# Kernel tuning notes

Hardware: AMD Instinct MI355X
Metric: run time of the kernel (lower is better)

The kernel has to match this reference:

```python
import jax, jax.numpy as jnp
import numpy as np

NB_CLASSES = 4
MRG = 0.05
ALPHA = 32.0
CL_W = 0.05
Z_PRUNE = 0.3
EPS = 1e-12


def _proxy_anchor(X, labels, valid, P):
    # X: [N, D] flattened span-pair features; labels: [N] int; valid: [N] float mask; P: [C, D]
    Xn = X / jnp.maximum(jnp.linalg.norm(X, axis=1, keepdims=True), EPS)
    Pn = P / jnp.maximum(jnp.linalg.norm(P, axis=1, keepdims=True), EPS)
    cos = Xn @ Pn.T  # [N, C]
    onehot = jax.nn.one_hot(labels, NB_CLASSES, dtype=cos.dtype)
    p_hot = onehot * valid[:, None]
    n_hot = (1.0 - onehot) * valid[:, None]
    pos_exp = jnp.exp(-ALPHA * (cos - MRG))
    neg_exp = jnp.exp(ALPHA * (cos + MRG))
    P_sim_sum = (p_hot * pos_exp).sum(axis=0)  # [C]
    N_sim_sum = (n_hot * neg_exp).sum(axis=0)  # [C]
    num_valid = jnp.maximum((p_hot.sum(axis=0) > 0).sum(), 1).astype(cos.dtype)
    pos_term = jnp.log1p(P_sim_sum).sum() / num_valid
    neg_term = jnp.log1p(N_sim_sum).sum() / NB_CLASSES
    return pos_term + neg_term


def _cl_loss(table, labels, attention_mask, P):
    B, L = table.shape[0], table.shape[1]
    lens = attention_mask.sum(axis=1)  # [B]
    idx = jnp.arange(L)
    rv = (idx[None, :] >= 1) & (idx[None, :] < (lens[:, None] - 1))  # [B, L]
    valid = (rv[:, :, None] & rv[:, None, :]).reshape(B, L * L).astype(table.dtype)
    X = table.reshape(B, L * L, -1)
    lab = labels.reshape(B, L * L)
    per_sample = jax.vmap(lambda x, l, v: _proxy_anchor(x, l, v, P))(X, lab, valid)
    return (CL_W * per_sample).mean()


def _span_pruning(pred, z, attention_mask):
    B = attention_mask.shape[0]
    mask_len = attention_mask.sum(axis=1) - 2
    length = (mask_len.astype(jnp.float32) * z).astype(jnp.int32)
    length = jnp.maximum(length, 10)
    length = jnp.minimum(length, mask_len * mask_len)
    pred_sort = -jnp.sort(-pred.reshape(B, -1), axis=1)  # descending
    topkth = pred_sort[jnp.arange(B), length - 1]
    return pred >= topkth[:, None, None]


def setup_inputs() -> dict:
    key = jax.random.key(0)
    ks = jax.random.split(key, 8)
    B, L, D = 4, 128, 768
    return {
        "table_edge": jax.random.normal(ks[0], (B, L, L, D), dtype=jnp.float32),
        "table_senti": jax.random.normal(ks[1], (B, L, L, D), dtype=jnp.float32),
        "attention_mask": jnp.ones((B, L), dtype=jnp.int32),
        "table_labels_S": jax.random.randint(ks[2], (B, L, L), 0, 2, dtype=jnp.int32),
        "table_labels_E": jax.random.randint(ks[3], (B, L, L), 0, 2, dtype=jnp.int32),
        "labels_edge": jax.random.randint(ks[4], (B, L, L), 0, 4, dtype=jnp.int32),
        "labels_senti": jax.random.randint(ks[5], (B, L, L), 0, 4, dtype=jnp.int32),
        "proxies_edge": jax.random.normal(ks[6], (4, D), dtype=jnp.float32),
        "proxies_senti": jax.random.normal(ks[7], (4, D), dtype=jnp.float32),
        "w_S": jax.random.normal(jax.random.fold_in(key, 10), (D,), dtype=jnp.float32) * 0.02,
        "b_S": jnp.zeros((1,), dtype=jnp.float32),
        "w_E": jax.random.normal(jax.random.fold_in(key, 11), (D,), dtype=jnp.float32) * 0.02,
        "b_E": jnp.zeros((1,), dtype=jnp.float32),
        "ID": 1,
        "epoch": 1,
    }


def reference(table_edge, table_senti, attention_mask, table_labels_S, table_labels_E,
              labels_edge, labels_senti, proxies_edge, proxies_senti,
              w_S, b_S, w_E, b_E, ID, epoch):
    cl_edge = _cl_loss(table_edge, labels_edge, attention_mask, proxies_edge)
    cl_senti = _cl_loss(table_senti, labels_senti, attention_mask, proxies_senti)

    logits_S = jnp.einsum('blmd,d->blm', table_edge, w_S) + b_S[0]
    logits_E = jnp.einsum('blmd,d->blm', table_edge, w_E) + b_E[0]

    weight = (table_labels_S >= 0).astype(logits_S.dtype)
    tS = table_labels_S.astype(logits_S.dtype)
    tE = table_labels_E.astype(logits_E.dtype)
    # BCEWithLogits: softplus(x) - x*t, weighted, mean over all elements
    loss_S = (weight * (jax.nn.softplus(logits_S) - logits_S * tS)).mean()
    loss_E = (weight * (jax.nn.softplus(logits_E) - logits_E * tE)).mean()

    S_pred = jax.nn.sigmoid(logits_S) * weight
    E_pred = jax.nn.sigmoid(logits_E) * weight
    pred_S = _span_pruning(S_pred, Z_PRUNE, attention_mask)
    pred_E = _span_pruning(E_pred, Z_PRUNE, attention_mask)

    return cl_edge, cl_senti, loss_S, loss_E, pred_S, pred_E
```

## Files before the change

kernel.cpp:

```cpp
#include <hip/hip_runtime.h>
#include <math.h>

#define LSEQ 128
#define NLL 16384
#define NBATCH 4
#define DIM 768
#define NB 4
#define ALPHA_C 32.0f
#define MRG_C 0.05f
#define CLW_C 0.05f
#define BPB 256
#define KS 24

__device__ __forceinline__ float wave_reduce_f(float v) {
#pragma unroll
    for (int s = 1; s < 64; s <<= 1) v += __shfl_xor(v, s);
    return v;
}

__device__ __forceinline__ float dot4(float4 a, float4 b) {
    return a.x*b.x + a.y*b.y + a.z*b.z + a.w*b.w;
}

template<bool EDGE>
__device__ __forceinline__ void kloop2(const float* __restrict__ rp0,
                                       const float* __restrict__ rp1,
                                       const float* __restrict__ wlds, int sub,
                                       float& xx0, float& d00, float& d01, float& d02, float& d03,
                                       float& dS0, float& dE0,
                                       float& xx1, float& d10, float& d11, float& d12, float& d13,
                                       float& dS1, float& dE1)
{
#pragma unroll 4
    for (int k = 0; k < KS; ++k) {
        const int off = k*32 + sub*4;
        const float4 x0 = *reinterpret_cast<const float4*>(rp0 + off);
        const float4 x1 = *reinterpret_cast<const float4*>(rp1 + off);
        const float4 w0 = *reinterpret_cast<const float4*>(&wlds[0*DIM + off]);
        const float4 w1 = *reinterpret_cast<const float4*>(&wlds[1*DIM + off]);
        const float4 w2 = *reinterpret_cast<const float4*>(&wlds[2*DIM + off]);
        const float4 w3 = *reinterpret_cast<const float4*>(&wlds[3*DIM + off]);
        xx0 += dot4(x0,x0); d00 += dot4(x0,w0); d01 += dot4(x0,w1); d02 += dot4(x0,w2); d03 += dot4(x0,w3);
        xx1 += dot4(x1,x1); d10 += dot4(x1,w0); d11 += dot4(x1,w1); d12 += dot4(x1,w2); d13 += dot4(x1,w3);
        if constexpr (EDGE) {
            const float4 w4 = *reinterpret_cast<const float4*>(&wlds[4*DIM + off]);
            const float4 w5 = *reinterpret_cast<const float4*>(&wlds[5*DIM + off]);
            dS0 += dot4(x0,w4); dE0 += dot4(x0,w5);
            dS1 += dot4(x1,w4); dE1 += dot4(x1,w5);
        }
    }
}

__global__ __launch_bounds__(256)
void fused_pass(const float* __restrict__ tabE, const float* __restrict__ tabS,
                const int* __restrict__ labE, const int* __restrict__ labSen,
                const int* __restrict__ attn,
                const float* __restrict__ proxE, const float* __restrict__ proxSen,
                const float* __restrict__ wS, const float* __restrict__ bS,
                const float* __restrict__ wE, const float* __restrict__ bE,
                const int* __restrict__ tlabS, const int* __restrict__ tlabE,
                float* __restrict__ pS, float* __restrict__ pE,
                float* __restrict__ partE, float* __restrict__ partSen)
{
    __shared__ float wlds[6*DIM];
    __shared__ float red[7*64];

    const int tid = threadIdx.x, wib = tid >> 6, lane = tid & 63;
    const int tbl = blockIdx.x >> 10;
    const int g = blockIdx.x & 1023;
    const int row0 = g << 6;
    const int b = g >> 8;
    const bool EDGE = (tbl == 0);

    const float* table = EDGE ? tabE : tabS;
    const float* prox  = EDGE ? proxE : proxSen;
    const int NW = EDGE ? 6 : 4;

    for (int i2 = tid; i2 < NW*192; i2 += 256) {
        const int v = i2 / 192, e = (i2 % 192) * 4;
        const float* src = (v < 4) ? (prox + v*DIM + e) : ((v == 4) ? (wS + e) : (wE + e));
        *reinterpret_cast<float4*>(&wlds[v*DIM + e]) = *reinterpret_cast<const float4*>(src);
    }
    __syncthreads();

    const int rgrp = lane >> 3, sub = lane & 7;
    const int r0 = row0 + wib*16 + rgrp*2;
    const float* rp0 = table + (size_t)r0 * DIM;
    const float* rp1 = rp0 + DIM;

    float xx0=0,d00=0,d01=0,d02=0,d03=0,dS0=0,dE0=0;
    float xx1=0,d10=0,d11=0,d12=0,d13=0,dS1=0,dE1=0;
    if (EDGE) kloop2<true >(rp0,rp1,wlds,sub,xx0,d00,d01,d02,d03,dS0,dE0,xx1,d10,d11,d12,d13,dS1,dE1);
    else      kloop2<false>(rp0,rp1,wlds,sub,xx0,d00,d01,d02,d03,dS0,dE0,xx1,d10,d11,d12,d13,dS1,dE1);

#pragma unroll
    for (int s = 1; s < 8; s <<= 1) {
        xx0+=__shfl_xor(xx0,s); d00+=__shfl_xor(d00,s); d01+=__shfl_xor(d01,s);
        d02+=__shfl_xor(d02,s); d03+=__shfl_xor(d03,s); dS0+=__shfl_xor(dS0,s); dE0+=__shfl_xor(dE0,s);
        xx1+=__shfl_xor(xx1,s); d10+=__shfl_xor(d10,s); d11+=__shfl_xor(d11,s);
        d12+=__shfl_xor(d12,s); d13+=__shfl_xor(d13,s); dS1+=__shfl_xor(dS1,s); dE1+=__shfl_xor(dE1,s);
    }
    if (sub == 0) {
        const int rr = wib*16 + rgrp*2;
        *reinterpret_cast<float2*>(&red[0*64+rr]) = make_float2(xx0, xx1);
        *reinterpret_cast<float2*>(&red[1*64+rr]) = make_float2(d00, d10);
        *reinterpret_cast<float2*>(&red[2*64+rr]) = make_float2(d01, d11);
        *reinterpret_cast<float2*>(&red[3*64+rr]) = make_float2(d02, d12);
        *reinterpret_cast<float2*>(&red[4*64+rr]) = make_float2(d03, d13);
        *reinterpret_cast<float2*>(&red[5*64+rr]) = make_float2(dS0, dS1);
        *reinterpret_cast<float2*>(&red[6*64+rr]) = make_float2(dE0, dE1);
    }
    __syncthreads();
    if (wib != 0) return;

    int lens_i = attn[b*LSEQ + lane] + attn[b*LSEQ + 64 + lane];
#pragma unroll
    for (int s = 1; s < 64; s <<= 1) lens_i += __shfl_xor(lens_i, s);

    float pinv[NB];
#pragma unroll
    for (int c = 0; c < NB; ++c) {
        float s2 = 0.f;
#pragma unroll
        for (int t = 0; t < 12; ++t) { const float w = wlds[c*DIM + t*64 + lane]; s2 += w*w; }
        s2 = wave_reduce_f(s2);
        pinv[c] = 1.0f / fmaxf(sqrtf(s2), 1e-12f);
    }

    const int r = row0 + lane;
    const float xx = red[lane];
    float dd[NB] = { red[64+lane], red[128+lane], red[192+lane], red[256+lane] };
    const float xinv = 1.0f / fmaxf(sqrtf(xx), 1e-12f);
    const int i = r & (NLL - 1);
    const int l = i >> 7, m = i & (LSEQ - 1);
    const bool valid = (l >= 1) && (l < lens_i - 1) && (m >= 1) && (m < lens_i - 1);
    const int lab = (EDGE ? labE : labSen)[r];

    float Pa[NB] = {0,0,0,0}, Na[NB] = {0,0,0,0}, Ca[NB] = {0,0,0,0};
    if (valid) {
#pragma unroll
        for (int c = 0; c < NB; ++c) {
            const float cs = dd[c] * xinv * pinv[c];
            if (lab == c) { Pa[c] = expf(-ALPHA_C * (cs - MRG_C)); Ca[c] = 1.f; }
            else          { Na[c] = expf( ALPHA_C * (cs + MRG_C)); }
        }
    }
    float sBS = 0.f, sBE = 0.f;
    if (EDGE) {
        const float dS = red[320+lane], dE = red[384+lane];
        const float xSl = dS + bS[0], xEl = dE + bE[0];
        const int ls = tlabS[r], le = tlabE[r];
        const float w = (ls >= 0) ? 1.f : 0.f;
        const float spS = fmaxf(xSl, 0.f) + log1pf(expf(-fabsf(xSl)));
        const float spE = fmaxf(xEl, 0.f) + log1pf(expf(-fabsf(xEl)));
        sBS = w * (spS - xSl * (float)ls);
        sBE = w * (spE - xEl * (float)le);
        pS[r] = w / (1.f + expf(-xSl));
        pE[r] = w / (1.f + expf(-xEl));
    }

#pragma unroll
    for (int c = 0; c < NB; ++c) {
        Pa[c] = wave_reduce_f(Pa[c]); Na[c] = wave_reduce_f(Na[c]); Ca[c] = wave_reduce_f(Ca[c]);
    }
    sBS = wave_reduce_f(sBS); sBE = wave_reduce_f(sBE);

    if (lane == 0) {
        float* pp = EDGE ? partE : partSen;
        const int blk = g & (BPB - 1);
        const int base = b * 14;
#pragma unroll
        for (int c = 0; c < NB; ++c) {
            pp[(base + c)     * BPB + blk] = Pa[c];
            pp[(base + 4 + c) * BPB + blk] = Na[c];
            pp[(base + 8 + c) * BPB + blk] = Ca[c];
        }
        pp[(base + 12) * BPB + blk] = sBS;
        pp[(base + 13) * BPB + blk] = sBE;
    }
}

__global__ __launch_bounds__(1024)
void tail_k(const float* __restrict__ pS, const float* __restrict__ pE,
            const int* __restrict__ attn,
            const float* __restrict__ partE, const float* __restrict__ partS,
            float* __restrict__ out)
{
    __shared__ unsigned sh[NLL];
    __shared__ int csum[16];
    __shared__ float gg[56];
    const int tid = threadIdx.x, wave = tid >> 6, lane = tid & 63;

    if (blockIdx.x >= 8) {
        const int tbl = blockIdx.x - 8;
        const float* part = (tbl == 0) ? partE : partS;
        for (int grp = wave; grp < 56; grp += 16) {
            float s = 0.f;
#pragma unroll
            for (int j = lane; j < BPB; j += 64) s += part[grp*BPB + j];
            s = wave_reduce_f(s);
            if (lane == 0) gg[grp] = s;
        }
        __syncthreads();
        if (tid == 0) {
            float tot = 0.f;
            for (int b = 0; b < NBATCH; ++b) {
                const float* G = gg + b * 14;
                int nv = 0;
                for (int c = 0; c < NB; ++c) nv += (G[8+c] > 0.f) ? 1 : 0;
                const float nvf = (float)((nv > 1) ? nv : 1);
                float pos = 0.f, neg = 0.f;
                for (int c = 0; c < NB; ++c) { pos += log1pf(G[c]); neg += log1pf(G[4+c]); }
                tot += pos / nvf + neg * 0.25f;
            }
            out[tbl] = CLW_C * tot * 0.25f;
            if (tbl == 0) {
                float bs = 0.f, be = 0.f;
                for (int b = 0; b < NBATCH; ++b) { bs += gg[b*14 + 12]; be += gg[b*14 + 13]; }
                out[2] = bs * (1.0f / 65536.0f);
                out[3] = be * (1.0f / 65536.0f);
            }
        }
        return;
    }

    const int a = blockIdx.x >> 2;
    const int b = blockIdx.x & 3;
    const float* p = (a ? pE : pS) + (size_t)b * NLL;
    float* o = out + 4 + (size_t)a * (NBATCH * NLL) + (size_t)b * NLL;

    int asum = attn[b*LSEQ + lane] + attn[b*LSEQ + 64 + lane];
#pragma unroll
    for (int s = 1; s < 64; s <<= 1) asum += __shfl_xor(asum, s);
    const int mask_len = asum - 2;
    int k = (int)((float)mask_len * 0.3f);
    k = (k > 10) ? k : 10;
    const int ml2 = mask_len * mask_len;
    k = (k < ml2) ? k : ml2;

    for (int j = tid; j < NLL; j += 1024) sh[j] = __float_as_uint(p[j]);
    __syncthreads();

    unsigned lo = 0u, hi = 0xFFFFFFFFu;
    for (int it = 0; it < 32; ++it) {
        if (lo >= hi) break;
        const unsigned span = hi - lo;
        const unsigned mid = lo + (span >> 1) + (span & 1u);
        int c = 0;
        for (int j = tid; j < NLL; j += 1024) c += (sh[j] >= mid) ? 1 : 0;
#pragma unroll
        for (int s = 1; s < 64; s <<= 1) c += __shfl_xor(c, s);
        if (lane == 0) csum[wave] = c;
        __syncthreads();
        int tot = 0;
#pragma unroll
        for (int w = 0; w < 16; ++w) tot += csum[w];
        if (tot >= k) lo = mid; else hi = mid - 1u;
        __syncthreads();
    }

    for (int j = tid; j < NLL; j += 1024) o[j] = (sh[j] >= lo) ? 1.0f : 0.0f;
}

extern "C" void kernel_launch(void* const* d_in, const int* in_sizes, int n_in,
                              void* d_out, int out_size, void* d_ws, size_t ws_size,
                              hipStream_t stream)
{
    const float* table_edge  = (const float*)d_in[0];
    const float* table_senti = (const float*)d_in[1];
    const int*   attn        = (const int*)d_in[2];
    const int*   tlabS       = (const int*)d_in[3];
    const int*   tlabE       = (const int*)d_in[4];
    const int*   lab_edge    = (const int*)d_in[5];
    const int*   lab_senti   = (const int*)d_in[6];
    const float* prox_edge   = (const float*)d_in[7];
    const float* prox_senti  = (const float*)d_in[8];
    const float* w_S         = (const float*)d_in[9];
    const float* b_S         = (const float*)d_in[10];
    const float* w_E         = (const float*)d_in[11];
    const float* b_E         = (const float*)d_in[12];

    float* out   = (float*)d_out;
    float* ws    = (float*)d_ws;
    float* pS    = ws;
    float* pE    = ws + 65536;
    float* partE = ws + 131072;
    float* partS = partE + 14336;

    fused_pass<<<2048, 256, 0, stream>>>(table_edge, table_senti,
        lab_edge, lab_senti, attn, prox_edge, prox_senti,
        w_S, b_S, w_E, b_E, tlabS, tlabE, pS, pE, partE, partS);
    tail_k<<<10, 1024, 0, stream>>>(pS, pE, attn, partE, partS, out);
}
```

Before: 109.4 us.

## Process four rows per lane group, 128 rows per block, per-wave epilogue

Each 8-lane group now accumulates four rows instead of two, so each block covers 128 rows and the grid halves to 1024 blocks. Edge and senti blocks are interleaved by block index. The post-processing now runs in every wave on its own 32 rows, and the four waves' partial sums are combined through shared memory before one write per block. The aim is to reuse each LDS weight load across more rows and to spread the epilogue across all waves instead of one. In exchange, register pressure is higher (launch bounds now request 4 blocks per SM) and there are fewer blocks to hide memory latency.

New measurement: 126.2 us. 1.15x slower.

```diff
diff --git a/kernel.cpp b/kernel.cpp
--- a/kernel.cpp
+++ b/kernel.cpp
@@ -9,7 +9,7 @@
 #define ALPHA_C 32.0f
 #define MRG_C 0.05f
 #define CLW_C 0.05f
-#define BPB 256
+#define BPB 128
 #define KS 24
 
 __device__ __forceinline__ float wave_reduce_f(float v) {
@@ -23,35 +23,41 @@
 }
 
 template<bool EDGE>
-__device__ __forceinline__ void kloop2(const float* __restrict__ rp0,
-                                       const float* __restrict__ rp1,
+__device__ __forceinline__ void kloop4(const float* __restrict__ rp,
                                        const float* __restrict__ wlds, int sub,
-                                       float& xx0, float& d00, float& d01, float& d02, float& d03,
-                                       float& dS0, float& dE0,
-                                       float& xx1, float& d10, float& d11, float& d12, float& d13,
-                                       float& dS1, float& dE1)
+                                       float (&xx)[4], float (&d0)[4], float (&d1)[4],
+                                       float (&d2)[4], float (&d3)[4],
+                                       float (&dS)[4], float (&dE)[4])
 {
-#pragma unroll 4
+#pragma unroll 2
     for (int k = 0; k < KS; ++k) {
         const int off = k*32 + sub*4;
-        const float4 x0 = *reinterpret_cast<const float4*>(rp0 + off);
-        const float4 x1 = *reinterpret_cast<const float4*>(rp1 + off);
+        float4 x[4];
+#pragma unroll
+        for (int rr = 0; rr < 4; ++rr)
+            x[rr] = *reinterpret_cast<const float4*>(rp + (size_t)rr*DIM + off);
         const float4 w0 = *reinterpret_cast<const float4*>(&wlds[0*DIM + off]);
         const float4 w1 = *reinterpret_cast<const float4*>(&wlds[1*DIM + off]);
         const float4 w2 = *reinterpret_cast<const float4*>(&wlds[2*DIM + off]);
         const float4 w3 = *reinterpret_cast<const float4*>(&wlds[3*DIM + off]);
-        xx0 += dot4(x0,x0); d00 += dot4(x0,w0); d01 += dot4(x0,w1); d02 += dot4(x0,w2); d03 += dot4(x0,w3);
-        xx1 += dot4(x1,x1); d10 += dot4(x1,w0); d11 += dot4(x1,w1); d12 += dot4(x1,w2); d13 += dot4(x1,w3);
+        float4 w4, w5;
         if constexpr (EDGE) {
-            const float4 w4 = *reinterpret_cast<const float4*>(&wlds[4*DIM + off]);
-            const float4 w5 = *reinterpret_cast<const float4*>(&wlds[5*DIM + off]);
-            dS0 += dot4(x0,w4); dE0 += dot4(x0,w5);
-            dS1 += dot4(x1,w4); dE1 += dot4(x1,w5);
-        }
-    }
-}
-
-__global__ __launch_bounds__(256)
+            w4 = *reinterpret_cast<const float4*>(&wlds[4*DIM + off]);
+            w5 = *reinterpret_cast<const float4*>(&wlds[5*DIM + off]);
+        }
+#pragma unroll
+        for (int rr = 0; rr < 4; ++rr) {
+            xx[rr] += dot4(x[rr], x[rr]);
+            d0[rr] += dot4(x[rr], w0);
+            d1[rr] += dot4(x[rr], w1);
+            d2[rr] += dot4(x[rr], w2);
+            d3[rr] += dot4(x[rr], w3);
+            if constexpr (EDGE) { dS[rr] += dot4(x[rr], w4); dE[rr] += dot4(x[rr], w5); }
+        }
+    }
+}
+
+__global__ __launch_bounds__(256, 4)
 void fused_pass(const float* __restrict__ tabE, const float* __restrict__ tabS,
                 const int* __restrict__ labE, const int* __restrict__ labSen,
                 const int* __restrict__ attn,
@@ -63,13 +69,14 @@
                 float* __restrict__ partE, float* __restrict__ partSen)
 {
     __shared__ float wlds[6*DIM];
-    __shared__ float red[7*64];
+    __shared__ float red[4][7*32];
+    __shared__ float sacc[4][14];
 
     const int tid = threadIdx.x, wib = tid >> 6, lane = tid & 63;
-    const int tbl = blockIdx.x >> 10;
-    const int g = blockIdx.x & 1023;
-    const int row0 = g << 6;
-    const int b = g >> 8;
+    const int tbl = blockIdx.x & 1;
+    const int g = blockIdx.x >> 1;
+    const int row0 = g << 7;
+    const int b = g >> 7;
     const bool EDGE = (tbl == 0);
 
     const float* table = EDGE ? tabE : tabS;
@@ -83,40 +90,9 @@
     }
     __syncthreads();
 
-    const int rgrp = lane >> 3, sub = lane & 7;
-    const int r0 = row0 + wib*16 + rgrp*2;
-    const float* rp0 = table + (size_t)r0 * DIM;
-    const float* rp1 = rp0 + DIM;
-
-    float xx0=0,d00=0,d01=0,d02=0,d03=0,dS0=0,dE0=0;
-    float xx1=0,d10=0,d11=0,d12=0,d13=0,dS1=0,dE1=0;
-    if (EDGE) kloop2<true >(rp0,rp1,wlds,sub,xx0,d00,d01,d02,d03,dS0,dE0,xx1,d10,d11,d12,d13,dS1,dE1);
-    else      kloop2<false>(rp0,rp1,wlds,sub,xx0,d00,d01,d02,d03,dS0,dE0,xx1,d10,d11,d12,d13,dS1,dE1);
-
-#pragma unroll
-    for (int s = 1; s < 8; s <<= 1) {
-        xx0+=__shfl_xor(xx0,s); d00+=__shfl_xor(d00,s); d01+=__shfl_xor(d01,s);
-        d02+=__shfl_xor(d02,s); d03+=__shfl_xor(d03,s); dS0+=__shfl_xor(dS0,s); dE0+=__shfl_xor(dE0,s);
-        xx1+=__shfl_xor(xx1,s); d10+=__shfl_xor(d10,s); d11+=__shfl_xor(d11,s);
-        d12+=__shfl_xor(d12,s); d13+=__shfl_xor(d13,s); dS1+=__shfl_xor(dS1,s); dE1+=__shfl_xor(dE1,s);
-    }
-    if (sub == 0) {
-        const int rr = wib*16 + rgrp*2;
-        *reinterpret_cast<float2*>(&red[0*64+rr]) = make_float2(xx0, xx1);
-        *reinterpret_cast<float2*>(&red[1*64+rr]) = make_float2(d00, d10);
-        *reinterpret_cast<float2*>(&red[2*64+rr]) = make_float2(d01, d11);
-        *reinterpret_cast<float2*>(&red[3*64+rr]) = make_float2(d02, d12);
-        *reinterpret_cast<float2*>(&red[4*64+rr]) = make_float2(d03, d13);
-        *reinterpret_cast<float2*>(&red[5*64+rr]) = make_float2(dS0, dS1);
-        *reinterpret_cast<float2*>(&red[6*64+rr]) = make_float2(dE0, dE1);
-    }
-    __syncthreads();
-    if (wib != 0) return;
-
     int lens_i = attn[b*LSEQ + lane] + attn[b*LSEQ + 64 + lane];
 #pragma unroll
     for (int s = 1; s < 64; s <<= 1) lens_i += __shfl_xor(lens_i, s);
-
     float pinv[NB];
 #pragma unroll
     for (int c = 0; c < NB; ++c) {
@@ -127,56 +103,95 @@
         pinv[c] = 1.0f / fmaxf(sqrtf(s2), 1e-12f);
     }
 
-    const int r = row0 + lane;
-    const float xx = red[lane];
-    float dd[NB] = { red[64+lane], red[128+lane], red[192+lane], red[256+lane] };
-    const float xinv = 1.0f / fmaxf(sqrtf(xx), 1e-12f);
-    const int i = r & (NLL - 1);
-    const int l = i >> 7, m = i & (LSEQ - 1);
-    const bool valid = (l >= 1) && (l < lens_i - 1) && (m >= 1) && (m < lens_i - 1);
-    const int lab = (EDGE ? labE : labSen)[r];
-
-    float Pa[NB] = {0,0,0,0}, Na[NB] = {0,0,0,0}, Ca[NB] = {0,0,0,0};
-    if (valid) {
-#pragma unroll
-        for (int c = 0; c < NB; ++c) {
-            const float cs = dd[c] * xinv * pinv[c];
-            if (lab == c) { Pa[c] = expf(-ALPHA_C * (cs - MRG_C)); Ca[c] = 1.f; }
-            else          { Na[c] = expf( ALPHA_C * (cs + MRG_C)); }
-        }
-    }
+    const int rgrp = lane >> 3, sub = lane & 7;
+    const int rbase = row0 + wib*32 + rgrp*4;
+    const float* rp = table + (size_t)rbase * DIM;
+
+    float xx[4]={0,0,0,0}, d0[4]={0,0,0,0}, d1[4]={0,0,0,0}, d2[4]={0,0,0,0},
+          d3[4]={0,0,0,0}, dS[4]={0,0,0,0}, dE[4]={0,0,0,0};
+    if (EDGE) kloop4<true >(rp, wlds, sub, xx, d0, d1, d2, d3, dS, dE);
+    else      kloop4<false>(rp, wlds, sub, xx, d0, d1, d2, d3, dS, dE);
+
+#pragma unroll
+    for (int s = 1; s < 8; s <<= 1) {
+#pragma unroll
+        for (int rr = 0; rr < 4; ++rr) {
+            xx[rr] += __shfl_xor(xx[rr], s);
+            d0[rr] += __shfl_xor(d0[rr], s); d1[rr] += __shfl_xor(d1[rr], s);
+            d2[rr] += __shfl_xor(d2[rr], s); d3[rr] += __shfl_xor(d3[rr], s);
+        }
+        if (EDGE) {
+#pragma unroll
+            for (int rr = 0; rr < 4; ++rr) {
+                dS[rr] += __shfl_xor(dS[rr], s); dE[rr] += __shfl_xor(dE[rr], s);
+            }
+        }
+    }
+    if (sub == 0) {
+        float* rw = red[wib];
+        const int rb = rgrp*4;
+        *reinterpret_cast<float4*>(&rw[0*32+rb]) = make_float4(xx[0],xx[1],xx[2],xx[3]);
+        *reinterpret_cast<float4*>(&rw[1*32+rb]) = make_float4(d0[0],d0[1],d0[2],d0[3]);
+        *reinterpret_cast<float4*>(&rw[2*32+rb]) = make_float4(d1[0],d1[1],d1[2],d1[3]);
+        *reinterpret_cast<float4*>(&rw[3*32+rb]) = make_float4(d2[0],d2[1],d2[2],d2[3]);
+        *reinterpret_cast<float4*>(&rw[4*32+rb]) = make_float4(d3[0],d3[1],d3[2],d3[3]);
+        if (EDGE) {
+            *reinterpret_cast<float4*>(&rw[5*32+rb]) = make_float4(dS[0],dS[1],dS[2],dS[3]);
+            *reinterpret_cast<float4*>(&rw[6*32+rb]) = make_float4(dE[0],dE[1],dE[2],dE[3]);
+        }
+    }
+    asm volatile("s_waitcnt lgkmcnt(0)" ::: "memory");
+
+    float Pa[NB]={0,0,0,0}, Na[NB]={0,0,0,0}, Ca[NB]={0,0,0,0};
     float sBS = 0.f, sBE = 0.f;
-    if (EDGE) {
-        const float dS = red[320+lane], dE = red[384+lane];
-        const float xSl = dS + bS[0], xEl = dE + bE[0];
-        const int ls = tlabS[r], le = tlabE[r];
-        const float w = (ls >= 0) ? 1.f : 0.f;
-        const float spS = fmaxf(xSl, 0.f) + log1pf(expf(-fabsf(xSl)));
-        const float spE = fmaxf(xEl, 0.f) + log1pf(expf(-fabsf(xEl)));
-        sBS = w * (spS - xSl * (float)ls);
-        sBE = w * (spE - xEl * (float)le);
-        pS[r] = w / (1.f + expf(-xSl));
-        pE[r] = w / (1.f + expf(-xEl));
-    }
-
+    if (lane < 32) {
+        const int r = row0 + wib*32 + lane;
+        const float* rw = red[wib];
+        const float xxv = rw[lane];
+        float dd[NB] = { rw[32+lane], rw[64+lane], rw[96+lane], rw[128+lane] };
+        const float xinv = 1.0f / fmaxf(sqrtf(xxv), 1e-12f);
+        const int i = r & (NLL - 1);
+        const int l = i >> 7, m = i & (LSEQ - 1);
+        const bool valid = (l >= 1) && (l < lens_i - 1) && (m >= 1) && (m < lens_i - 1);
+        const int lab = (EDGE ? labE : labSen)[r];
+        if (valid) {
+#pragma unroll
+            for (int c = 0; c < NB; ++c) {
+                const float cs = dd[c] * xinv * pinv[c];
+                if (lab == c) { Pa[c] = expf(-ALPHA_C * (cs - MRG_C)); Ca[c] = 1.f; }
+                else          { Na[c] = expf( ALPHA_C * (cs + MRG_C)); }
+            }
+        }
+        if (EDGE) {
+            const float dSl = rw[160+lane], dEl = rw[192+lane];
+            const float xSl = dSl + bS[0], xEl = dEl + bE[0];
+            const int ls = tlabS[r], le = tlabE[r];
+            const float w = (ls >= 0) ? 1.f : 0.f;
+            const float spS = fmaxf(xSl, 0.f) + log1pf(expf(-fabsf(xSl)));
+            const float spE = fmaxf(xEl, 0.f) + log1pf(expf(-fabsf(xEl)));
+            sBS = w * (spS - xSl * (float)ls);
+            sBE = w * (spE - xEl * (float)le);
+            pS[r] = w / (1.f + expf(-xSl));
+            pE[r] = w / (1.f + expf(-xEl));
+        }
+    }
 #pragma unroll
     for (int c = 0; c < NB; ++c) {
         Pa[c] = wave_reduce_f(Pa[c]); Na[c] = wave_reduce_f(Na[c]); Ca[c] = wave_reduce_f(Ca[c]);
     }
     sBS = wave_reduce_f(sBS); sBE = wave_reduce_f(sBE);
-
     if (lane == 0) {
+        float* sp = sacc[wib];
+#pragma unroll
+        for (int c = 0; c < NB; ++c) { sp[c] = Pa[c]; sp[4+c] = Na[c]; sp[8+c] = Ca[c]; }
+        sp[12] = sBS; sp[13] = sBE;
+    }
+    __syncthreads();
+    if (tid < 14) {
+        const float s = sacc[0][tid] + sacc[1][tid] + sacc[2][tid] + sacc[3][tid];
         float* pp = EDGE ? partE : partSen;
         const int blk = g & (BPB - 1);
-        const int base = b * 14;
-#pragma unroll
-        for (int c = 0; c < NB; ++c) {
-            pp[(base + c)     * BPB + blk] = Pa[c];
-            pp[(base + 4 + c) * BPB + blk] = Na[c];
-            pp[(base + 8 + c) * BPB + blk] = Ca[c];
-        }
-        pp[(base + 12) * BPB + blk] = sBS;
-        pp[(base + 13) * BPB + blk] = sBE;
+        pp[(b * 14 + tid) * BPB + blk] = s;
     }
 }
 
@@ -285,9 +300,9 @@
     float* pS    = ws;
     float* pE    = ws + 65536;
     float* partE = ws + 131072;
-    float* partS = partE + 14336;
-
-    fused_pass<<<2048, 256, 0, stream>>>(table_edge, table_senti,
+    float* partS = partE + 7168;
+
+    fused_pass<<<1024, 256, 0, stream>>>(table_edge, table_senti,
         lab_edge, lab_senti, attn, prox_edge, prox_senti,
         w_S, b_S, w_E, b_E, tlabS, tlabE, pS, pE, partE, partS);
     tail_k<<<10, 1024, 0, stream>>>(pS, pE, attn, partE, partS, out);
```
